# Performance work log

Hardware: AMD Instinct MI355X
Metric: run time of the kernel (lower is better)

The kernel has to match this reference:

```python
import jax, jax.numpy as jnp
import numpy as np

B, CIN, COUT, SDIM, H, W, K = 16, 512, 512, 512, 32, 32, 3
LIN_SCALE = 1.0 / np.sqrt(SDIM)            # EqualLinear equalized-lr scale
CONV_SCALE = 1.0 / np.sqrt(CIN * K * K)    # ModulatedConv2d equalized-lr scale
ACT_GAIN = np.sqrt(2.0)                    # EqualLeakyReLU gain
NEG_SLOPE = 0.2
EPS = 1e-8


def setup_inputs() -> dict:
    key = jax.random.key(0)
    ks = jax.random.split(key, 6)
    x = jax.random.normal(ks[0], (B, CIN, H, W), jnp.float32)
    w = jax.random.normal(ks[1], (B, SDIM), jnp.float32)
    noise = jax.random.normal(ks[2], (B, 1, 2 * H, 2 * W), jnp.float32)
    lin_w = jax.random.normal(ks[3], (CIN, SDIM), jnp.float32)
    lin_b = jnp.ones((CIN,), jnp.float32)  # nn.init.ones_(self.style.bias)
    conv_w = jax.random.normal(ks[4], (COUT, CIN, K, K), jnp.float32)
    noise_weight = jnp.float32(0.1)  # scalar noise strength (nonzero so the noise path is exercised)
    return {"x": x, "w": w, "noise": noise, "lin_w": lin_w, "lin_b": lin_b,
            "conv_w": conv_w, "noise_weight": noise_weight}


def reference(x, w, noise, lin_w, lin_b, conv_w, noise_weight):
    b, c, h, wd = x.shape
    x = jax.image.resize(x, (b, c, 2 * h, 2 * wd), method="bilinear")
    # 2) style = EqualLinear(w): [B, CIN]
    s = w @ (lin_w * LIN_SCALE).T + lin_b
    # 3) modulated conv: modulate input, shared-weight conv, demodulate output
    wk = conv_w * CONV_SCALE                       # [COUT, CIN, K, K]
    xm = x * s[:, :, None, None]                   # per-sample input modulation
    y = jax.lax.conv_general_dilated(
        xm, wk, window_strides=(1, 1), padding=((1, 1), (1, 1)),
        dimension_numbers=("NCHW", "OIHW", "NCHW"))
    # demod[b,o] = 1/sqrt(sum_{i,k,l} (wk[o,i,k,l]*s[b,i])^2 + eps)
    demod = jax.lax.rsqrt(jnp.einsum("oikl,bi->bo", wk * wk, s * s) + EPS)
    y = y * demod[:, :, None, None]
    # 4) noise injection + equalized leaky relu
    y = y + noise_weight * noise
    return jnp.where(y >= 0, y, NEG_SLOPE * y) * ACT_GAIN
```

## Files before the change

### kernel.cpp

```cpp
#include <hip/hip_runtime.h>
#include <hip/hip_bf16.h>
#include <string.h>

#define B_ 16
#define CIN_ 512
#define COUT_ 512
#define SDIM_ 512
#define HIN_ 32
#define WIN_ 32
#define HOUT_ 64
#define WOUT_ 64

#define LIN_SCALE_C 0.044194173824159216f
#define CONV_SCALE_C 0.014731391274719742f

typedef short short8 __attribute__((ext_vector_type(8)));
typedef float f32x4 __attribute__((ext_vector_type(4)));

typedef const __attribute__((address_space(1))) void* gptr_t;
typedef __attribute__((address_space(3))) void* sptr_t;

#define GLDS0(SRC, DST) \
    __builtin_amdgcn_global_load_lds((gptr_t)(SRC), (sptr_t)(DST), 16, 0, 0)

__global__ void style_kernel(const float* __restrict__ w, const float* __restrict__ lin_w,
                             const float* __restrict__ lin_b, float* __restrict__ s) {
    const int gw   = (blockIdx.x * 256 + threadIdx.x) >> 6;
    const int lane = threadIdx.x & 63;
    const int b = gw >> 9, i = gw & 511;
    const float* wr = w + b * SDIM_;
    const float* lw = lin_w + i * SDIM_;
    float acc = 0.f;
    #pragma unroll
    for (int j = 0; j < 8; ++j) acc += wr[lane + j * 64] * lw[lane + j * 64];
    #pragma unroll
    for (int off = 32; off; off >>= 1) acc += __shfl_xor(acc, off);
    if (lane == 0) s[b * CIN_ + i] = acc * LIN_SCALE_C + lin_b[i];
}

__global__ void prep_weights(const float* __restrict__ conv_w, __hip_bfloat16* __restrict__ w2,
                             float* __restrict__ wsq, float* __restrict__ zbuf) {
    __shared__ float xs[4608];
    const int o = blockIdx.x;
    const int tid = threadIdx.x;
    for (int idx = tid; idx < 4608; idx += 256) xs[idx] = conv_w[o * 4608 + idx];
    __syncthreads();
    for (int i = tid; i < CIN_; i += 256) {
        float ss = 0.f;
        #pragma unroll
        for (int kk = 0; kk < 9; ++kk) {
            float v = xs[i * 9 + kk] * CONV_SCALE_C;
            ss += v * v;
            w2[o * 4608 + kk * 512 + i] = __float2bfloat16(v);
        }
        wsq[o * CIN_ + i] = ss;
    }
    if (blockIdx.x == 0 && tid < 256) zbuf[tid] = 0.f;
}

__global__ void demod_kernel(const float* __restrict__ wsq, const float* __restrict__ s,
                             float* __restrict__ demod) {
    const int gw   = (blockIdx.x * 256 + threadIdx.x) >> 6;
    const int lane = threadIdx.x & 63;
    const int b = gw >> 9, o = gw & 511;
    const float* sr = s + b * CIN_;
    const float* wr = wsq + o * CIN_;
    float acc = 0.f;
    #pragma unroll
    for (int j = 0; j < 8; ++j) {
        float sv = sr[lane + j * 64];
        acc += wr[lane + j * 64] * sv * sv;
    }
    #pragma unroll
    for (int off = 32; off; off >>= 1) acc += __shfl_xor(acc, off);
    if (lane == 0) demod[b * COUT_ + o] = 1.0f / sqrtf(acc + 1e-8f);
}

__global__ void upsample_mod_kernel(const float* __restrict__ x, const float* __restrict__ s,
                                    __hip_bfloat16* __restrict__ xq) {
    __shared__ float xs[10 * 32 * 33];
    __shared__ float ssh[32];
    const int ht = blockIdx.x;
    const int ct = blockIdx.y;
    const int b  = blockIdx.z;
    const int tid = threadIdx.x;
    const int ho0 = ht * 16, h0 = ht * 8, c0 = ct * 32;

    if (tid < 32) ssh[tid] = s[b * CIN_ + c0 + tid];
    for (int idx = tid; idx < 10240; idx += 256) {
        int ch = idx / 320; int rem = idx - ch * 320;
        int rr = rem >> 5;  int col = rem & 31;
        int srow = h0 - 1 + rr; srow = min(max(srow, 0), 31);
        xs[(rr * 32 + col) * 33 + ch] = x[((b * CIN_ + c0 + ch) * HIN_ + srow) * WIN_ + col];
    }
    __syncthreads();

    for (int e = tid; e < 4096; e += 256) {
        int c8 = e & 3; int wo = (e >> 2) & 63; int hr = e >> 8;
        int ri0 = (hr + (hr & 1)) >> 1;
        float wlo_h = (hr & 1) ? 0.75f : 0.25f;
        int clo = (wo - 2 + (wo & 1)) >> 1;
        float wlo_w = (wo & 1) ? 0.75f : 0.25f;
        int chi = min(clo + 1, 31); clo = max(clo, 0);
        const float* r0p = xs + (ri0 * 32) * 33;
        const float* r1p = xs + ((ri0 + 1) * 32) * 33;
        short8 v;
        #pragma unroll
        for (int q = 0; q < 8; ++q) {
            const int c = c8 * 8 + q;
            float v0 = r0p[clo * 33 + c];
            float v1 = r0p[chi * 33 + c];
            float v2 = r1p[clo * 33 + c];
            float v3 = r1p[chi * 33 + c];
            float rlo = wlo_w * v0 + (1.f - wlo_w) * v1;
            float rhi = wlo_w * v2 + (1.f - wlo_w) * v3;
            float val = (wlo_h * rlo + (1.f - wlo_h) * rhi) * ssh[c];
            __hip_bfloat16 hv = __float2bfloat16(val);
            unsigned short us;
            __builtin_memcpy(&us, &hv, 2);
            v[q] = (short)us;
        }
        *(short8*)(xq + (((size_t)(b * 64) + ho0 + hr) * 64 + wo) * 512 + c0 + c8 * 8) = v;
    }
}

__global__ __launch_bounds__(512)
void conv_kernel(const __hip_bfloat16* __restrict__ xq,
                 const __hip_bfloat16* __restrict__ w2,
                 const float* __restrict__ demod,
                 const float* __restrict__ noise,
                 const float* __restrict__ nw_p,
                 float* __restrict__ out,
                 const __hip_bfloat16* __restrict__ zbuf) {
    extern __shared__ __hip_bfloat16 smem[];
    __hip_bfloat16* As = smem;
    __hip_bfloat16* Bs = smem + 32768;

    const int bid = blockIdx.x;
    const int swz = (bid & 7) * 64 + (bid >> 3);
    const int b  = swz >> 5;
    const int mt = (swz >> 4) & 1;
    const int nt = swz & 15;
    const int o0 = mt * 256;
    const int p0 = nt * 256;

    const int tid  = threadIdx.x;
    const int lane = tid & 63;
    const int wave = tid >> 6;
    const int wm = wave >> 2, wn = wave & 3;

    const int srow = tid >> 2;
    const int schk = (((tid & 3) ^ ((tid >> 3) & 3))) * 8;
    const int aoff = (o0 + srow) * 4608 + schk;
    const int brow_lo = nt * 4 + (srow >> 6);
    const int bcol = srow & 63;
    const int sdst = tid * 8;

    const int lrow = lane & 15;
    const int pko = ((lane >> 4) ^ ((lrow >> 1) & 3)) * 8;
    const int ard = (wm * 128 + lrow) * 32 + pko;
    const int brd = (wn * 64 + lrow) * 32 + pko;

    const __hip_bfloat16* Ar = As + ard;
    const __hip_bfloat16* Br = Bs + brd;
    __hip_bfloat16* Ad = As + sdst;
    __hip_bfloat16* Bd = Bs + sdst;
    const __hip_bfloat16* aB0 = w2 + aoff;
    const __hip_bfloat16* aB1 = aB0 + 589824;

    f32x4 acc[8][4] = {};

    #define MKB(DH, DW, H) \
        ((((unsigned)(brow_lo + (H) * 2 + (DH)) < 64u) && ((unsigned)(bcol + (DW)) < 64u)) \
            ? xq + (size_t)((b * 64 + brow_lo + (H) * 2 + (DH)) * 64 + (bcol + (DW))) * 512 + schk \
            : zbuf)

    const __hip_bfloat16* pB0c = MKB(-1, -1, 0);
    const __hip_bfloat16* pB1c = MKB(-1, -1, 1);

    GLDS0(aB0,       Ad);        GLDS0(aB1,       Ad + 4096);
    GLDS0(pB0c,      Bd);        GLDS0(pB1c,      Bd + 4096);
    GLDS0(aB0 + 32,  Ad + 8192); GLDS0(aB1 + 32,  Ad + 8192 + 4096);
    GLDS0(pB0c + 32, Bd + 8192); GLDS0(pB1c + 32, Bd + 8192 + 4096);
    asm volatile("s_waitcnt vmcnt(0)" ::: "memory");
    __builtin_amdgcn_s_barrier();

    #define MR(AV, MI) \
        acc[MI][0] = __builtin_amdgcn_mfma_f32_16x16x32_bf16(AV, b0_, acc[MI][0], 0, 0, 0); \
        acc[MI][1] = __builtin_amdgcn_mfma_f32_16x16x32_bf16(AV, b1_, acc[MI][1], 0, 0, 0); \
        acc[MI][2] = __builtin_amdgcn_mfma_f32_16x16x32_bf16(AV, b2_, acc[MI][2], 0, 0, 0); \
        acc[MI][3] = __builtin_amdgcn_mfma_f32_16x16x32_bf16(AV, b3_, acc[MI][3], 0, 0, 0)

    #define WINB(V) do { \
        short8 a0_ = *(const short8*)(Ar + ((V) & 3) * 8192 + 0 * 512); \
        short8 a1_ = *(const short8*)(Ar + ((V) & 3) * 8192 + 1 * 512); \
        short8 a2_ = *(const short8*)(Ar + ((V) & 3) * 8192 + 2 * 512); \
        short8 a3_ = *(const short8*)(Ar + ((V) & 3) * 8192 + 3 * 512); \
        short8 a4_ = *(const short8*)(Ar + ((V) & 3) * 8192 + 4 * 512); \
        short8 a5_ = *(const short8*)(Ar + ((V) & 3) * 8192 + 5 * 512); \
        short8 a6_ = *(const short8*)(Ar + ((V) & 3) * 8192 + 6 * 512); \
        short8 a7_ = *(const short8*)(Ar + ((V) & 3) * 8192 + 7 * 512); \
        short8 b0_ = *(const short8*)(Br + ((V) & 3) * 8192 + 0 * 512); \
        short8 b1_ = *(const short8*)(Br + ((V) & 3) * 8192 + 1 * 512); \
        short8 b2_ = *(const short8*)(Br + ((V) & 3) * 8192 + 2 * 512); \
        short8 b3_ = *(const short8*)(Br + ((V) & 3) * 8192 + 3 * 512); \
        __builtin_amdgcn_s_setprio(1); \
        MR(a0_, 0); MR(a1_, 1); MR(a2_, 2); MR(a3_, 3); \
        MR(a4_, 4); MR(a5_, 5); MR(a6_, 6); MR(a7_, 7); \
        __builtin_amdgcn_s_setprio(0); \
    } while (0)

    #define STG(U, PB0, PB1) do { \
        GLDS0(aB0 + (U) * 32,           Ad + ((U) & 3) * 8192); \
        GLDS0(aB1 + (U) * 32,           Ad + ((U) & 3) * 8192 + 4096); \
        GLDS0((PB0) + ((U) & 15) * 32,  Bd + ((U) & 3) * 8192); \
        GLDS0((PB1) + ((U) & 15) * 32,  Bd + ((U) & 3) * 8192 + 4096); \
    } while (0)

    #define PAIR(V) do { \
        if ((V) <= 12) { \
            STG((V) + 2, pB0c, pB1c); \
            STG((V) + 3, pB0c, pB1c); \
        } else if (kk < 8) {            \
            STG((V) + 2, pB0n, pB1n); \
            STG((V) + 3, pB0n, pB1n); \
        } \
        WINB(V); \
        WINB((V) + 1); \
        asm volatile("s_waitcnt vmcnt(0)" ::: "memory"); \
        __builtin_amdgcn_s_barrier(); \
    } while (0)

    #pragma unroll 1
    for (int kk = 0; kk < 9; ++kk) {
        const int kn  = kk + 1;
        const int kdn = (kn * 11) >> 5;
        const int dhn = kdn - 1, dwn = kn - kdn * 3 - 1;
        const __hip_bfloat16* pB0n = MKB(dhn, dwn, 0);
        const __hip_bfloat16* pB1n = MKB(dhn, dwn, 1);

        PAIR(0);  PAIR(2);  PAIR(4);  PAIR(6);
        PAIR(8);  PAIR(10); PAIR(12); PAIR(14);

        pB0c = pB0n; pB1c = pB1n;
        aB0 += 512;  aB1 += 512;
    }
    #undef PAIR
    #undef STG
    #undef WINB
    #undef MR
    #undef MKB

    const float nwv = nw_p[0];
    const int colp = lane & 15;
    const int rgrp = (lane >> 4) * 4;
    float nz[4];
    #pragma unroll
    for (int ni = 0; ni < 4; ++ni)
        nz[ni] = noise[b * 4096 + p0 + wn * 64 + ni * 16 + colp] * nwv;
    #pragma unroll
    for (int mi = 0; mi < 8; ++mi) {
        const int obase = o0 + wm * 128 + mi * 16 + rgrp;
        float dm[4];
        #pragma unroll
        for (int j = 0; j < 4; ++j) dm[j] = demod[b * COUT_ + obase + j];
        #pragma unroll
        for (int ni = 0; ni < 4; ++ni) {
            const int pix = p0 + wn * 64 + ni * 16 + colp;
            #pragma unroll
            for (int j = 0; j < 4; ++j) {
                float v = acc[mi][ni][j] * dm[j] + nz[ni];
                v = (v >= 0.f ? v : 0.2f * v) * 1.4142135623730951f;
                out[(b * COUT_ + obase + j) * 4096 + pix] = v;
            }
        }
    }
}

extern "C" void kernel_launch(void* const* d_in, const int* in_sizes, int n_in,
                              void* d_out, int out_size, void* d_ws, size_t ws_size,
                              hipStream_t stream) {
    const float* x      = (const float*)d_in[0];
    const float* w      = (const float*)d_in[1];
    const float* noise  = (const float*)d_in[2];
    const float* lin_w  = (const float*)d_in[3];
    const float* lin_b  = (const float*)d_in[4];
    const float* conv_w = (const float*)d_in[5];
    const float* nw     = (const float*)d_in[6];
    float* out = (float*)d_out;

    char* ws = (char*)d_ws;
    __hip_bfloat16* xq = (__hip_bfloat16*)ws;
    __hip_bfloat16* w2 = (__hip_bfloat16*)(ws + 67108864);
    float* s     = (float*)(ws + 71827456);
    float* demod = (float*)(ws + 71860224);
    float* wsq   = (float*)(ws + 71892992);
    float* zbuf  = (float*)(ws + 72941568);

    static int lds_set = 0;
    if (!lds_set) {
        (void)hipFuncSetAttribute((const void*)conv_kernel,
                                  hipFuncAttributeMaxDynamicSharedMemorySize, 131072);
        lds_set = 1;
    }

    style_kernel<<<2048, 256, 0, stream>>>(w, lin_w, lin_b, s);
    prep_weights<<<512, 256, 0, stream>>>(conv_w, w2, wsq, zbuf);
    demod_kernel<<<2048, 256, 0, stream>>>(wsq, s, demod);
    upsample_mod_kernel<<<dim3(4, 16, 16), 256, 0, stream>>>(x, s, xq);
    conv_kernel<<<512, 512, 131072, stream>>>(xq, w2, demod, noise, nw, out,
                                              (const __hip_bfloat16*)zbuf);
}
```

Measured before the change: 292.6 us.

## Double-buffer LDS fragment reads and use a finer-grained vmcnt pipeline per k-window

The main loop changes from processing pairs of k-windows with a full vmcnt(0) drain into a per-window pipeline. Each step issues one stage of global-to-LDS loads, waits only until 4 loads remain outstanding, and barriers. It then reads the next window's A/B fragments from LDS into a second register set while running the MFMAs on the current set. The goal is to hide LDS read latency behind MFMA work and avoid draining all global loads each step, at the cost of one barrier per window instead of per pair and 96 extra VGPRs for fragment double-buffering, which may cut occupancy.

```diff
diff --git a/kernel.cpp b/kernel.cpp
--- a/kernel.cpp
+++ b/kernel.cpp
@@ -169,6 +169,7 @@
     const __hip_bfloat16* aB1 = aB0 + 589824;
 
     f32x4 acc[8][4] = {};
+    short8 fA[12], fB[12];
 
     #define MKB(DH, DW, H) \
         ((((unsigned)(brow_lo + (H) * 2 + (DH)) < 64u) && ((unsigned)(bcol + (DW)) < 64u)) \
@@ -177,38 +178,6 @@
 
     const __hip_bfloat16* pB0c = MKB(-1, -1, 0);
     const __hip_bfloat16* pB1c = MKB(-1, -1, 1);
-
-    GLDS0(aB0,       Ad);        GLDS0(aB1,       Ad + 4096);
-    GLDS0(pB0c,      Bd);        GLDS0(pB1c,      Bd + 4096);
-    GLDS0(aB0 + 32,  Ad + 8192); GLDS0(aB1 + 32,  Ad + 8192 + 4096);
-    GLDS0(pB0c + 32, Bd + 8192); GLDS0(pB1c + 32, Bd + 8192 + 4096);
-    asm volatile("s_waitcnt vmcnt(0)" ::: "memory");
-    __builtin_amdgcn_s_barrier();
-
-    #define MR(AV, MI) \
-        acc[MI][0] = __builtin_amdgcn_mfma_f32_16x16x32_bf16(AV, b0_, acc[MI][0], 0, 0, 0); \
-        acc[MI][1] = __builtin_amdgcn_mfma_f32_16x16x32_bf16(AV, b1_, acc[MI][1], 0, 0, 0); \
-        acc[MI][2] = __builtin_amdgcn_mfma_f32_16x16x32_bf16(AV, b2_, acc[MI][2], 0, 0, 0); \
-        acc[MI][3] = __builtin_amdgcn_mfma_f32_16x16x32_bf16(AV, b3_, acc[MI][3], 0, 0, 0)
-
-    #define WINB(V) do { \
-        short8 a0_ = *(const short8*)(Ar + ((V) & 3) * 8192 + 0 * 512); \
-        short8 a1_ = *(const short8*)(Ar + ((V) & 3) * 8192 + 1 * 512); \
-        short8 a2_ = *(const short8*)(Ar + ((V) & 3) * 8192 + 2 * 512); \
-        short8 a3_ = *(const short8*)(Ar + ((V) & 3) * 8192 + 3 * 512); \
-        short8 a4_ = *(const short8*)(Ar + ((V) & 3) * 8192 + 4 * 512); \
-        short8 a5_ = *(const short8*)(Ar + ((V) & 3) * 8192 + 5 * 512); \
-        short8 a6_ = *(const short8*)(Ar + ((V) & 3) * 8192 + 6 * 512); \
-        short8 a7_ = *(const short8*)(Ar + ((V) & 3) * 8192 + 7 * 512); \
-        short8 b0_ = *(const short8*)(Br + ((V) & 3) * 8192 + 0 * 512); \
-        short8 b1_ = *(const short8*)(Br + ((V) & 3) * 8192 + 1 * 512); \
-        short8 b2_ = *(const short8*)(Br + ((V) & 3) * 8192 + 2 * 512); \
-        short8 b3_ = *(const short8*)(Br + ((V) & 3) * 8192 + 3 * 512); \
-        __builtin_amdgcn_s_setprio(1); \
-        MR(a0_, 0); MR(a1_, 1); MR(a2_, 2); MR(a3_, 3); \
-        MR(a4_, 4); MR(a5_, 5); MR(a6_, 6); MR(a7_, 7); \
-        __builtin_amdgcn_s_setprio(0); \
-    } while (0)
 
     #define STG(U, PB0, PB1) do { \
         GLDS0(aB0 + (U) * 32,           Ad + ((U) & 3) * 8192); \
@@ -217,19 +186,55 @@
         GLDS0((PB1) + ((U) & 15) * 32,  Bd + ((U) & 3) * 8192 + 4096); \
     } while (0)
 
-    #define PAIR(V) do { \
-        if ((V) <= 12) { \
+    #define READS(V1, NXT) do { \
+        const __hip_bfloat16* Ap_ = Ar + ((V1) & 3) * 8192; \
+        const __hip_bfloat16* Bp_ = Br + ((V1) & 3) * 8192; \
+        NXT[0]  = *(const short8*)(Ap_ + 0 * 512); \
+        NXT[1]  = *(const short8*)(Ap_ + 1 * 512); \
+        NXT[2]  = *(const short8*)(Ap_ + 2 * 512); \
+        NXT[3]  = *(const short8*)(Ap_ + 3 * 512); \
+        NXT[4]  = *(const short8*)(Ap_ + 4 * 512); \
+        NXT[5]  = *(const short8*)(Ap_ + 5 * 512); \
+        NXT[6]  = *(const short8*)(Ap_ + 6 * 512); \
+        NXT[7]  = *(const short8*)(Ap_ + 7 * 512); \
+        NXT[8]  = *(const short8*)(Bp_ + 0 * 512); \
+        NXT[9]  = *(const short8*)(Bp_ + 1 * 512); \
+        NXT[10] = *(const short8*)(Bp_ + 2 * 512); \
+        NXT[11] = *(const short8*)(Bp_ + 3 * 512); \
+    } while (0)
+
+    #define MFMAS(CUR) do { \
+        __builtin_amdgcn_s_setprio(1); \
+        _Pragma("unroll") \
+        for (int mi_ = 0; mi_ < 8; ++mi_) { \
+            _Pragma("unroll") \
+            for (int ni_ = 0; ni_ < 4; ++ni_) \
+                acc[mi_][ni_] = __builtin_amdgcn_mfma_f32_16x16x32_bf16( \
+                    CUR[mi_], CUR[8 + ni_], acc[mi_][ni_], 0, 0, 0); \
+        } \
+        __builtin_amdgcn_s_setprio(0); \
+    } while (0)
+
+    #define WIN(V, CUR, NXT) do { \
+        if ((V) < 14) { \
             STG((V) + 2, pB0c, pB1c); \
-            STG((V) + 3, pB0c, pB1c); \
-        } else if (kk < 8) {            \
+            asm volatile("s_waitcnt vmcnt(4)" ::: "memory"); \
+        } else if (kk < 8) { \
             STG((V) + 2, pB0n, pB1n); \
-            STG((V) + 3, pB0n, pB1n); \
+            asm volatile("s_waitcnt vmcnt(4)" ::: "memory"); \
+        } else { \
+            asm volatile("s_waitcnt vmcnt(0)" ::: "memory"); \
         } \
-        WINB(V); \
-        WINB((V) + 1); \
-        asm volatile("s_waitcnt vmcnt(0)" ::: "memory"); \
         __builtin_amdgcn_s_barrier(); \
+        if ((V) < 15 || kk < 8) READS((V) + 1, NXT); \
+        MFMAS(CUR); \
     } while (0)
+
+    STG(0, pB0c, pB1c);
+    STG(1, pB0c, pB1c);
+    asm volatile("s_waitcnt vmcnt(4)" ::: "memory");
+    __builtin_amdgcn_s_barrier();
+    READS(0, fA);
 
     #pragma unroll 1
     for (int kk = 0; kk < 9; ++kk) {
@@ -239,16 +244,18 @@
         const __hip_bfloat16* pB0n = MKB(dhn, dwn, 0);
         const __hip_bfloat16* pB1n = MKB(dhn, dwn, 1);
 
-        PAIR(0);  PAIR(2);  PAIR(4);  PAIR(6);
-        PAIR(8);  PAIR(10); PAIR(12); PAIR(14);
+        WIN(0,  fA, fB); WIN(1,  fB, fA); WIN(2,  fA, fB); WIN(3,  fB, fA);
+        WIN(4,  fA, fB); WIN(5,  fB, fA); WIN(6,  fA, fB); WIN(7,  fB, fA);
+        WIN(8,  fA, fB); WIN(9,  fB, fA); WIN(10, fA, fB); WIN(11, fB, fA);
+        WIN(12, fA, fB); WIN(13, fB, fA); WIN(14, fA, fB); WIN(15, fB, fA);
 
         pB0c = pB0n; pB1c = pB1n;
         aB0 += 512;  aB1 += 512;
     }
-    #undef PAIR
+    #undef WIN
+    #undef MFMAS
+    #undef READS
     #undef STG
-    #undef WINB
-    #undef MR
     #undef MKB
 
     const float nwv = nw_p[0];
```

New measurement: 549.7 us. +87.8%, slower.
